# Kernel tuning notes

Hardware: AMD Instinct MI355X
Metric: run time of the kernel (lower is better)

The kernel has to match this reference:

```python
import jax, jax.numpy as jnp
import numpy as np

N_COMP = 16  # sedenion components

def _cd_table(n):
    """Cayley-Dickson basis multiplication table: e_i * e_j = sign[i,j] * e_{idx[i,j]}."""
    if n == 1:
        return np.array([[1]], dtype=np.int64), np.array([[0]], dtype=np.int64)
    m = n // 2
    s, k = _cd_table(m)
    conj = np.where(np.arange(m) == 0, 1, -1)  # conj(e_0)=e_0, conj(e_i)=-e_i
    S = np.zeros((n, n), dtype=np.int64)
    K = np.zeros((n, n), dtype=np.int64)
    for i in range(n):
        for j in range(n):
            if i < m and j < m:          # (a,0)(c,0) = (ac, 0)
                S[i, j] = s[i, j]; K[i, j] = k[i, j]
            elif i < m:                  # (a,0)(0,d) = (0, d a)
                q = j - m
                S[i, j] = s[q, i]; K[i, j] = m + k[q, i]
            elif j < m:                  # (0,b)(c,0) = (0, b c*)
                p = i - m
                S[i, j] = s[p, j] * conj[j]; K[i, j] = m + k[p, j]
            else:                        # (0,b)(0,d) = (-d* b, 0)
                p, q = i - m, j - m
                S[i, j] = -conj[q] * s[q, p]; K[i, j] = k[q, p]
    return S, K

SIGN, IDX = _cd_table(N_COMP)

def _sedenion_kernel(w_comp):
    """Assemble the (16n, 16n) real matrix of the sedenion linear map from 16 (n,n) component weights."""
    blocks = [[None] * N_COMP for _ in range(N_COMP)]
    for i in range(N_COMP):
        for j in range(N_COMP):
            blocks[j][int(IDX[i, j])] = float(SIGN[i, j]) * w_comp[i]
    return jnp.concatenate([jnp.concatenate(row, axis=1) for row in blocks], axis=0)


def setup_inputs() -> dict:
    key = jax.random.key(0)
    k1, k2, k3, k4 = jax.random.split(key, 4)
    B, C, H, W = 8, 96, 256, 256
    x = jax.random.normal(k1, (B, C, H, W), jnp.float32)
    w_comp = jax.random.normal(k2, (N_COMP, C, C), jnp.float32) * 0.02
    proj_w = jax.random.normal(k3, (C, C), jnp.float32) * 0.02
    proj_b = jax.random.normal(k4, (C,), jnp.float32) * 0.02
    return {"x": x, "w_comp": w_comp, "proj_w": proj_w, "proj_b": proj_b}


def reference(x, w_comp, proj_w, proj_b):
    B, C, H, W = x.shape
    h, w = H // 4, W // 4
    # get_window: 'b c (h s1) (w s2) -> b h w (s1 s2 c)' with s1=s2=4
    xw = x.reshape(B, C, h, 4, w, 4).transpose(0, 2, 4, 3, 5, 1).reshape(B, h, w, 16 * C)
    big = _sedenion_kernel(w_comp)          # (16C, 16C)
    y = xw @ big                            # sedenion linear on windowed features
    # reverse_window + 'b c h w -> b h w c' fused: (B,h,w,16C) -> (B,H,W,C)
    y = y.reshape(B, h, w, 4, 4, C).transpose(0, 1, 3, 2, 4, 5).reshape(B, H, W, C)
    y = jax.nn.gelu(y, approximate=False)   # nn.GELU (exact); dropouts are identity (p=0)
    y = y @ proj_w.T + proj_b               # nn.Linear(dim, dim)
    return y.transpose(0, 3, 1, 2)          # 'b h w c -> b c h w'
```

## Files before the change

### kernel.cpp

```cpp
#include <hip/hip_runtime.h>
#include <hip/hip_bf16.h>

typedef __attribute__((ext_vector_type(8))) short short8v;
typedef __attribute__((ext_vector_type(4))) float float4v;

struct SedTab { signed char sgn[256]; signed char idx[256]; };

__device__ inline unsigned short f2bf(float f) {
    __hip_bfloat16 h = __float2bfloat16(f);
    return *reinterpret_cast<unsigned short*>(&h);
}
__device__ inline float bf2f(unsigned short u) {
    union { unsigned int i; float f; } x; x.i = ((unsigned)u) << 16; return x.f;
}

#define GLOAD_LDS16(g, l) __builtin_amdgcn_global_load_lds( \
    (const __attribute__((address_space(1))) void*)(g), \
    (__attribute__((address_space(3))) void*)(l), 16, 0, 0)

#define VMCNT(n) asm volatile("s_waitcnt vmcnt(" #n ")" ::: "memory")

__global__ __launch_bounds__(256) void build_bigT(
    const float* __restrict__ w_comp, unsigned short* __restrict__ bigT, SedTab tab)
{
    int e = blockIdx.x * 256 + threadIdx.x;
    if (e >= 1536 * 1536) return;
    int n = e / 1536, k = e - n * 1536;
    int t_out = n / 96, c = n - t_out * 96;
    int t_in = k / 96, m = k - t_in * 96;
    int i = tab.idx[t_in * 16 + t_out];
    float s = (float)tab.sgn[t_in * 16 + t_out];
    float v = s * w_comp[(i * 96 + m) * 96 + c];
    bigT[e] = f2bf(v);
}

__global__ __launch_bounds__(256) void window_cast(
    const float* __restrict__ x, unsigned short* __restrict__ xw)
{
    __shared__ unsigned short lds[96][260];
    int blk = blockIdx.x;
    int s1 = blk & 3, hh = (blk >> 2) & 63, b = blk >> 8;
    const float* src = x + (size_t)b * 6291456 + (size_t)(4 * hh + s1) * 256;

    for (int i = threadIdx.x; i < 6144; i += 256) {
        int m = i >> 6;
        int q = (i & 63) << 2;
        float4 v = *(const float4*)(src + (size_t)m * 65536 + q);
        lds[m][q + 0] = f2bf(v.x);
        lds[m][q + 1] = f2bf(v.y);
        lds[m][q + 2] = f2bf(v.z);
        lds[m][q + 3] = f2bf(v.w);
    }
    __syncthreads();
    size_t rowbase = (size_t)((b * 64 + hh) * 64) * 1536 + (size_t)s1 * 384;
    for (int i = threadIdx.x; i < 3072; i += 256) {
        int ww = i / 48, g = i - ww * 48;
        int s2 = g / 12, mg = (g - s2 * 12) * 8;
        int qq = 4 * ww + s2;
        short8v pk;
        #pragma unroll
        for (int j = 0; j < 8; ++j) pk[j] = (short)lds[mg + j][qq];
        *(short8v*)(xw + rowbase + (size_t)ww * 1536 + s2 * 96 + mg) = pk;
    }
}

__global__ __launch_bounds__(512, 2) void gemm_sed8(
    const unsigned short* __restrict__ A,
    const unsigned short* __restrict__ Bt,
    unsigned short* __restrict__ Yg)
{
    __shared__ unsigned short As[3][256 * 64];
    __shared__ unsigned short Bs[2][256 * 64];
    const int t = threadIdx.x;
    const int lane = t & 63, w = t >> 6;
    const int wm = w >> 2, wn = w & 3;
    const int lr = lane & 15, lg = lane >> 4;

    const int bid = blockIdx.x;
    const int wg = (bid & 7) * 96 + (bid >> 3);
    const int nt = wg >> 7, mt = wg & 127;
    const int m0 = mt * 256, n0 = nt * 256;

    float4v acc[8][4];
    #pragma unroll
    for (int i = 0; i < 8; ++i)
        #pragma unroll
        for (int j = 0; j < 4; ++j) acc[i][j] = (float4v)0.0f;

    auto stageA = [&](int kt, int half, int i) {
        const int c = t + i * 512;
        const int row = half * 128 + (c >> 3);
        const int kc = ((c & 7) ^ (row & 7)) << 3;
        GLOAD_LDS16(A + (size_t)(m0 + row) * 1536 + kt * 64 + kc,
                    (char*)&As[kt % 3][0] + half * 16384 + c * 16);
    };
    auto stageB = [&](int kt, int half, int i) {
        const int c = t + i * 512;
        const int row = half * 128 + (c >> 3);
        const int kc = ((c & 7) ^ (row & 7)) << 3;
        GLOAD_LDS16(Bt + (size_t)(n0 + row) * 1536 + kt * 64 + kc,
                    (char*)&Bs[kt & 1][0] + half * 16384 + c * 16);
    };

    stageA(0, 0, 0); stageA(0, 0, 1); stageA(0, 1, 0); stageA(0, 1, 1);
    stageB(0, 0, 0); stageB(0, 0, 1); stageB(0, 1, 0); stageB(0, 1, 1);
    stageA(1, 0, 0); stageA(1, 0, 1); stageA(1, 1, 0); stageA(1, 1, 1);
    VMCNT(4);
    __builtin_amdgcn_s_barrier();

    const int c0 = (lg * 8) ^ ((lr & 7) << 3);
    const int c1 = (32 + lg * 8) ^ ((lr & 7) << 3);

    for (int kt = 0; kt < 24; ++kt) {
        const unsigned short* as = &As[kt % 3][0];
        const unsigned short* bs = &Bs[kt & 1][0];
        const int arow0 = wm * 128 + lr;
        const int brow0 = wn * 64 + lr;

        short8v a0[4], b0[4];
        #pragma unroll
        for (int mf = 0; mf < 4; ++mf)
            a0[mf] = *(const short8v*)(as + (arow0 + mf * 16) * 64 + c0);
        #pragma unroll
        for (int nf = 0; nf < 4; ++nf)
            b0[nf] = *(const short8v*)(bs + (brow0 + nf * 16) * 64 + c0);
        if (kt < 23) { stageB(kt + 1, 0, 0); stageB(kt + 1, 0, 1); }
        __builtin_amdgcn_s_barrier();
        __builtin_amdgcn_s_setprio(1);
        #pragma unroll
        for (int mf = 0; mf < 4; ++mf)
            #pragma unroll
            for (int nf = 0; nf < 4; ++nf)
                acc[mf][nf] = __builtin_amdgcn_mfma_f32_16x16x32_bf16(
                    a0[mf], b0[nf], acc[mf][nf], 0, 0, 0);
        __builtin_amdgcn_s_setprio(0);
        __builtin_amdgcn_s_barrier();

        short8v a1[4];
        #pragma unroll
        for (int mf = 0; mf < 4; ++mf)
            a1[mf] = *(const short8v*)(as + (arow0 + 64 + mf * 16) * 64 + c0);
        if (kt < 23) { stageB(kt + 1, 1, 0); stageB(kt + 1, 1, 1); }
        __builtin_amdgcn_s_barrier();
        __builtin_amdgcn_s_setprio(1);
        #pragma unroll
        for (int mf = 0; mf < 4; ++mf)
            #pragma unroll
            for (int nf = 0; nf < 4; ++nf)
                acc[4 + mf][nf] = __builtin_amdgcn_mfma_f32_16x16x32_bf16(
                    a1[mf], b0[nf], acc[4 + mf][nf], 0, 0, 0);
        __builtin_amdgcn_s_setprio(0);
        __builtin_amdgcn_s_barrier();

        short8v a2[4], b1[4];
        #pragma unroll
        for (int mf = 0; mf < 4; ++mf)
            a2[mf] = *(const short8v*)(as + (arow0 + mf * 16) * 64 + c1);
        #pragma unroll
        for (int nf = 0; nf < 4; ++nf)
            b1[nf] = *(const short8v*)(bs + (brow0 + nf * 16) * 64 + c1);
        if (kt < 22) { stageA(kt + 2, 0, 0); stageA(kt + 2, 0, 1); }
        __builtin_amdgcn_s_barrier();
        __builtin_amdgcn_s_setprio(1);
        #pragma unroll
        for (int mf = 0; mf < 4; ++mf)
            #pragma unroll
            for (int nf = 0; nf < 4; ++nf)
                acc[mf][nf] = __builtin_amdgcn_mfma_f32_16x16x32_bf16(
                    a2[mf], b1[nf], acc[mf][nf], 0, 0, 0);
        __builtin_amdgcn_s_setprio(0);
        __builtin_amdgcn_s_barrier();

        short8v a3[4];
        #pragma unroll
        for (int mf = 0; mf < 4; ++mf)
            a3[mf] = *(const short8v*)(as + (arow0 + 64 + mf * 16) * 64 + c1);
        if (kt < 22) { stageA(kt + 2, 1, 0); stageA(kt + 2, 1, 1); }
        __builtin_amdgcn_s_barrier();
        __builtin_amdgcn_s_setprio(1);
        #pragma unroll
        for (int mf = 0; mf < 4; ++mf)
            #pragma unroll
            for (int nf = 0; nf < 4; ++nf)
                acc[4 + mf][nf] = __builtin_amdgcn_mfma_f32_16x16x32_bf16(
                    a3[mf], b1[nf], acc[4 + mf][nf], 0, 0, 0);
        __builtin_amdgcn_s_setprio(0);
        if (kt < 22)       { VMCNT(4); }
        else if (kt == 22) { VMCNT(0); }
        __builtin_amdgcn_s_barrier();
    }

    #pragma unroll
    for (int mf = 0; mf < 8; ++mf) {
        #pragma unroll
        for (int r = 0; r < 4; ++r) {
            const int gm = m0 + wm * 128 + mf * 16 + lg * 4 + r;
            #pragma unroll
            for (int nf = 0; nf < 4; ++nf) {
                const int gn = n0 + wn * 64 + nf * 16 + lr;
                float v = acc[mf][nf][r];
                float g = 0.5f * v * (1.0f + erff(v * 0.70710678118654752f));
                Yg[(size_t)gm * 1536 + gn] = f2bf(g);
            }
        }
    }
}

__global__ __launch_bounds__(256, 2) void proj_mfma(
    const unsigned short* __restrict__ Yg,
    const float* __restrict__ pw, const float* __restrict__ pb,
    float* __restrict__ out)
{
    __shared__ unsigned short gys[256 * 104];
    __shared__ unsigned short pws[96 * 104];
    __shared__ float pbs[96];

    const int blk = blockIdx.x;
    const int s1 = blk & 3, hh = (blk >> 2) & 63, b = blk >> 8;
    const int t = threadIdx.x;
    const int lane = t & 63, w = t >> 6;
    const int lr = lane & 15;

    for (int i = t; i < 9216; i += 256) {
        int r = i / 96, c = i - r * 96;
        pws[r * 104 + c] = f2bf(pw[i]);
    }
    if (t < 96) pbs[t] = pb[t];

    size_t rowbase = (size_t)((b * 64 + hh) * 64) * 1536 + (size_t)s1 * 384;
    for (int i = t; i < 3072; i += 256) {
        int ww = i / 48, v = i - ww * 48;
        short8v pk = *(const short8v*)(Yg + rowbase + (size_t)ww * 1536 + v * 8);
        int s2 = v / 12;
        int c = (v - s2 * 12) * 8;
        int q = 4 * ww + s2;
        *(short8v*)(&gys[q * 104 + c]) = pk;
    }
    __syncthreads();

    float4v acc[6][4];
    #pragma unroll
    for (int i = 0; i < 6; ++i)
        #pragma unroll
        for (int j = 0; j < 4; ++j) acc[i][j] = (float4v)0.0f;

    #pragma unroll
    for (int ks = 0; ks < 3; ++ks) {
        const int lk = ks * 32 + ((lane >> 4) << 3);
        short8v af[6], bf[4];
        #pragma unroll
        for (int mf = 0; mf < 6; ++mf)
            af[mf] = *(const short8v*)(&pws[(mf * 16 + lr) * 104 + lk]);
        #pragma unroll
        for (int nf = 0; nf < 4; ++nf)
            bf[nf] = *(const short8v*)(&gys[(w * 64 + nf * 16 + lr) * 104 + lk]);
        #pragma unroll
        for (int mf = 0; mf < 6; ++mf)
            #pragma unroll
            for (int nf = 0; nf < 4; ++nf)
                acc[mf][nf] = __builtin_amdgcn_mfma_f32_16x16x32_bf16(
                    af[mf], bf[nf], acc[mf][nf], 0, 0, 0);
    }

    const int p = 4 * hh + s1;
    const size_t obase = (size_t)b * 6291456 + (size_t)p * 256;
    #pragma unroll
    for (int mf = 0; mf < 6; ++mf) {
        #pragma unroll
        for (int r = 0; r < 4; ++r) {
            const int c = mf * 16 + (lane >> 4) * 4 + r;
            const float bias = pbs[c];
            #pragma unroll
            for (int nf = 0; nf < 4; ++nf) {
                const int q = w * 64 + nf * 16 + lr;
                out[obase + (size_t)c * 65536 + q] = acc[mf][nf][r] + bias;
            }
        }
    }
}

static void cd_table(int n, int* S, int* K) {
    if (n == 1) { S[0] = 1; K[0] = 0; return; }
    int m = n / 2;
    int s[64], k[64];
    cd_table(m, s, k);
    for (int i = 0; i < n; ++i) {
        for (int j = 0; j < n; ++j) {
            if (i < m && j < m) { S[i*n+j] = s[i*m+j]; K[i*n+j] = k[i*m+j]; }
            else if (i < m) { int q = j - m; S[i*n+j] = s[q*m+i]; K[i*n+j] = m + k[q*m+i]; }
            else if (j < m) { int p = i - m; int cj = (j == 0) ? 1 : -1;
                              S[i*n+j] = s[p*m+j] * cj; K[i*n+j] = m + k[p*m+j]; }
            else { int p = i - m, q = j - m; int cq = (q == 0) ? 1 : -1;
                   S[i*n+j] = -cq * s[q*m+p]; K[i*n+j] = k[q*m+p]; }
        }
    }
}

extern "C" void kernel_launch(void* const* d_in, const int* in_sizes, int n_in,
                              void* d_out, int out_size, void* d_ws, size_t ws_size,
                              hipStream_t stream) {
    const float* x      = (const float*)d_in[0];
    const float* w_comp = (const float*)d_in[1];
    const float* proj_w = (const float*)d_in[2];
    const float* proj_b = (const float*)d_in[3];
    float* out = (float*)d_out;

    unsigned short* BigT = (unsigned short*)d_ws;
    unsigned short* Yg   = (unsigned short*)((char*)d_ws + 4718592);
    unsigned short* Xw   = (unsigned short*)d_out;

    int S16[256], K16[256];
    cd_table(16, S16, K16);
    SedTab tab;
    for (int i = 0; i < 16; ++i)
        for (int j = 0; j < 16; ++j) {
            int k = K16[i * 16 + j];
            tab.idx[j * 16 + k] = (signed char)i;
            tab.sgn[j * 16 + k] = (signed char)S16[i * 16 + j];
        }

    hipLaunchKernelGGL(build_bigT, dim3(9216), dim3(256), 0, stream, w_comp, BigT, tab);
    hipLaunchKernelGGL(window_cast, dim3(2048), dim3(256), 0, stream, x, Xw);
    hipLaunchKernelGGL(gemm_sed8, dim3(768), dim3(512), 0, stream, Xw, BigT, Yg);
    hipLaunchKernelGGL(proj_mfma, dim3(2048), dim3(256), 0, stream, Yg, proj_w, proj_b, out);
}
```

Measured before the change: 347.4 us.

## Halve per-iteration barriers and hoist global staging addresses in bf16 GEMM

The main GEMM K-loop drops the trailing barrier after each of its four MFMA phases, keeping only the barrier before each phase. The vmcnt wait moves ahead of the last phase's barrier so the next tile's data is resident before the loop wraps. Global load addresses for A and B staging are now computed once outside the loop and advanced by a running k offset. LDS buffers are rotated through pointer swaps instead of `kt % 3` and `kt & 1` indexing. This cuts synchronization stalls and per-stage address arithmetic, but relies on the remaining barriers still ordering buffer reuse correctly across waves.

New measurement: 327.6 us. -5.7%, faster.

```diff
diff --git a/kernel.cpp b/kernel.cpp
--- a/kernel.cpp
+++ b/kernel.cpp
@@ -87,35 +87,43 @@
         #pragma unroll
         for (int j = 0; j < 4; ++j) acc[i][j] = (float4v)0.0f;
 
-    auto stageA = [&](int kt, int half, int i) {
-        const int c = t + i * 512;
-        const int row = half * 128 + (c >> 3);
-        const int kc = ((c & 7) ^ (row & 7)) << 3;
-        GLOAD_LDS16(A + (size_t)(m0 + row) * 1536 + kt * 64 + kc,
-                    (char*)&As[kt % 3][0] + half * 16384 + c * 16);
+    const int r0c = t >> 3,          r1c = (t + 512) >> 3;
+    const int kc0 = ((t & 7) ^ (r0c & 7)) << 3;
+    const int kc1 = (((t + 512) & 7) ^ (r1c & 7)) << 3;
+    const unsigned short* gA0 = A  + (size_t)(m0 + r0c) * 1536 + kc0;
+    const unsigned short* gA1 = A  + (size_t)(m0 + r1c) * 1536 + kc1;
+    const unsigned short* gB0 = Bt + (size_t)(n0 + r0c) * 1536 + kc0;
+    const unsigned short* gB1 = Bt + (size_t)(n0 + r1c) * 1536 + kc1;
+    const int d0 = t * 16, d1 = (t + 512) * 16;
+
+    auto stage2 = [&](const unsigned short* g0, const unsigned short* g1,
+                      char* ldst, int ko, int half) {
+        GLOAD_LDS16(g0 + ko + half * 196608, ldst + half * 16384 + d0);
+        GLOAD_LDS16(g1 + ko + half * 196608, ldst + half * 16384 + d1);
     };
-    auto stageB = [&](int kt, int half, int i) {
-        const int c = t + i * 512;
-        const int row = half * 128 + (c >> 3);
-        const int kc = ((c & 7) ^ (row & 7)) << 3;
-        GLOAD_LDS16(Bt + (size_t)(n0 + row) * 1536 + kt * 64 + kc,
-                    (char*)&Bs[kt & 1][0] + half * 16384 + c * 16);
-    };
-
-    stageA(0, 0, 0); stageA(0, 0, 1); stageA(0, 1, 0); stageA(0, 1, 1);
-    stageB(0, 0, 0); stageB(0, 0, 1); stageB(0, 1, 0); stageB(0, 1, 1);
-    stageA(1, 0, 0); stageA(1, 0, 1); stageA(1, 1, 0); stageA(1, 1, 1);
+
+    char* a_rd = (char*)&As[0][0];
+    char* a_md = (char*)&As[0][0] + 32768;
+    char* a_wr = (char*)&As[0][0] + 65536;
+    char* b_rd = (char*)&Bs[0][0];
+    char* b_wr = (char*)&Bs[0][0] + 32768;
+
+    stage2(gA0, gA1, a_rd, 0, 0);  stage2(gA0, gA1, a_rd, 0, 1);
+    stage2(gB0, gB1, b_rd, 0, 0);  stage2(gB0, gB1, b_rd, 0, 1);
+    stage2(gA0, gA1, a_md, 64, 0); stage2(gA0, gA1, a_md, 64, 1);
     VMCNT(4);
     __builtin_amdgcn_s_barrier();
 
     const int c0 = (lg * 8) ^ ((lr & 7) << 3);
     const int c1 = (32 + lg * 8) ^ ((lr & 7) << 3);
+    const int arow0 = wm * 128 + lr;
+    const int brow0 = wn * 64 + lr;
+
+    int koB = 64, koA = 128;
 
     for (int kt = 0; kt < 24; ++kt) {
-        const unsigned short* as = &As[kt % 3][0];
-        const unsigned short* bs = &Bs[kt & 1][0];
-        const int arow0 = wm * 128 + lr;
-        const int brow0 = wn * 64 + lr;
+        const unsigned short* as = (const unsigned short*)a_rd;
+        const unsigned short* bs = (const unsigned short*)b_rd;
 
         short8v a0[4], b0[4];
         #pragma unroll
@@ -124,7 +132,7 @@
         #pragma unroll
         for (int nf = 0; nf < 4; ++nf)
             b0[nf] = *(const short8v*)(bs + (brow0 + nf * 16) * 64 + c0);
-        if (kt < 23) { stageB(kt + 1, 0, 0); stageB(kt + 1, 0, 1); }
+        if (kt < 23) stage2(gB0, gB1, b_wr, koB, 0);
         __builtin_amdgcn_s_barrier();
         __builtin_amdgcn_s_setprio(1);
         #pragma unroll
@@ -134,13 +142,12 @@
                 acc[mf][nf] = __builtin_amdgcn_mfma_f32_16x16x32_bf16(
                     a0[mf], b0[nf], acc[mf][nf], 0, 0, 0);
         __builtin_amdgcn_s_setprio(0);
-        __builtin_amdgcn_s_barrier();
 
         short8v a1[4];
         #pragma unroll
         for (int mf = 0; mf < 4; ++mf)
             a1[mf] = *(const short8v*)(as + (arow0 + 64 + mf * 16) * 64 + c0);
-        if (kt < 23) { stageB(kt + 1, 1, 0); stageB(kt + 1, 1, 1); }
+        if (kt < 23) stage2(gB0, gB1, b_wr, koB, 1);
         __builtin_amdgcn_s_barrier();
         __builtin_amdgcn_s_setprio(1);
         #pragma unroll
@@ -150,7 +157,6 @@
                 acc[4 + mf][nf] = __builtin_amdgcn_mfma_f32_16x16x32_bf16(
                     a1[mf], b0[nf], acc[4 + mf][nf], 0, 0, 0);
         __builtin_amdgcn_s_setprio(0);
-        __builtin_amdgcn_s_barrier();
 
         short8v a2[4], b1[4];
         #pragma unroll
@@ -159,7 +165,7 @@
         #pragma unroll
         for (int nf = 0; nf < 4; ++nf)
             b1[nf] = *(const short8v*)(bs + (brow0 + nf * 16) * 64 + c1);
-        if (kt < 22) { stageA(kt + 2, 0, 0); stageA(kt + 2, 0, 1); }
+        if (kt < 22) stage2(gA0, gA1, a_wr, koA, 0);
         __builtin_amdgcn_s_barrier();
         __builtin_amdgcn_s_setprio(1);
         #pragma unroll
@@ -169,13 +175,14 @@
                 acc[mf][nf] = __builtin_amdgcn_mfma_f32_16x16x32_bf16(
                     a2[mf], b1[nf], acc[mf][nf], 0, 0, 0);
         __builtin_amdgcn_s_setprio(0);
-        __builtin_amdgcn_s_barrier();
 
         short8v a3[4];
         #pragma unroll
         for (int mf = 0; mf < 4; ++mf)
             a3[mf] = *(const short8v*)(as + (arow0 + 64 + mf * 16) * 64 + c1);
-        if (kt < 22) { stageA(kt + 2, 1, 0); stageA(kt + 2, 1, 1); }
+        if (kt < 22) stage2(gA0, gA1, a_wr, koA, 1);
+        if (kt < 22)       { VMCNT(4); }
+        else if (kt == 22) { VMCNT(0); }
         __builtin_amdgcn_s_barrier();
         __builtin_amdgcn_s_setprio(1);
         #pragma unroll
@@ -185,9 +192,10 @@
                 acc[4 + mf][nf] = __builtin_amdgcn_mfma_f32_16x16x32_bf16(
                     a3[mf], b1[nf], acc[4 + mf][nf], 0, 0, 0);
         __builtin_amdgcn_s_setprio(0);
-        if (kt < 22)       { VMCNT(4); }
-        else if (kt == 22) { VMCNT(0); }
-        __builtin_amdgcn_s_barrier();
+
+        char* tmp = a_rd; a_rd = a_md; a_md = a_wr; a_wr = tmp;
+        tmp = b_rd; b_rd = b_wr; b_wr = tmp;
+        koB += 64; koA += 64;
     }
 
     #pragma unroll
```
